# Kernel optimization log

Measured on AMD Instinct MI355X. Metric: run time of the kernel, lower is better.

Reference implementation:

```python
import jax, jax.numpy as jnp
import numpy as np

N_NODES = 50000
N_EDGES = 800000
IN_CH = 128
OUT_CH = 64
HEADS = 2
NEG_SLOPE = 0.2


def _gat_conv(x, src, dst, W, a_src, a_dst, b, n):
    """PyG-style GATConv (eval mode: no dropout), self-loops already appended.
    x: [n, F_in]; W: [F_in, H*C]; a_src/a_dst: [H, C]; b: [H*C]."""
    H, C = a_src.shape
    h = (x @ W).reshape(n, H, C)                       # [n, H, C]
    alpha_src = jnp.sum(h * a_src, axis=-1)            # [n, H]
    alpha_dst = jnp.sum(h * a_dst, axis=-1)            # [n, H]
    e = alpha_src[src] + alpha_dst[dst]                # [E, H]
    e = jnp.where(e > 0, e, NEG_SLOPE * e)             # LeakyReLU(0.2)
    # neighbor-wise (destination-grouped) softmax, numerically stable
    m = jax.ops.segment_max(e, dst, num_segments=n)
    e = jnp.exp(e - m[dst])
    denom = jax.ops.segment_sum(e, dst, num_segments=n)
    alpha = e / (denom[dst] + 1e-16)                   # [E, H]
    out = jax.ops.segment_sum(alpha[:, :, None] * h[src], dst, num_segments=n)
    return out.reshape(n, H * C) + b


def setup_inputs() -> dict:
    key = jax.random.key(0)
    ks = jax.random.split(key, 12)
    s = 0.08  # glorot-ish scale
    x = jax.random.normal(ks[0], (N_NODES, IN_CH), dtype=jnp.float32)
    edge_index = jax.random.randint(ks[1], (2, N_EDGES), 0, N_NODES, dtype=jnp.int64)
    H, O = HEADS, OUT_CH
    return {
        "x": x,
        "edge_index": edge_index,
        "W1": jax.random.normal(ks[2], (IN_CH, H * 2 * O), dtype=jnp.float32) * s,
        "a_src1": jax.random.normal(ks[3], (H, 2 * O), dtype=jnp.float32) * s,
        "a_dst1": jax.random.normal(ks[4], (H, 2 * O), dtype=jnp.float32) * s,
        "b1": jnp.zeros((H * 2 * O,), dtype=jnp.float32),
        "W_mu": jax.random.normal(ks[5], (2 * O * H, H * O), dtype=jnp.float32) * s,
        "a_src_mu": jax.random.normal(ks[6], (H, O), dtype=jnp.float32) * s,
        "a_dst_mu": jax.random.normal(ks[7], (H, O), dtype=jnp.float32) * s,
        "b_mu": jnp.zeros((H * O,), dtype=jnp.float32),
        "W_ls": jax.random.normal(ks[8], (2 * O * H, H * O), dtype=jnp.float32) * s,
        "a_src_ls": jax.random.normal(ks[9], (H, O), dtype=jnp.float32) * s,
        "a_dst_ls": jax.random.normal(ks[10], (H, O), dtype=jnp.float32) * s,
        "b_ls": jnp.zeros((H * O,), dtype=jnp.float32),
    }


def reference(x, edge_index, W1, a_src1, a_dst1, b1,
              W_mu, a_src_mu, a_dst_mu, b_mu,
              W_ls, a_src_ls, a_dst_ls, b_ls):
    n = x.shape[0]
    loop = jnp.arange(n, dtype=edge_index.dtype)
    src = jnp.concatenate([edge_index[0], loop])  # PyG add_self_loops=True
    dst = jnp.concatenate([edge_index[1], loop])
    x1 = jax.nn.elu(_gat_conv(x, src, dst, W1, a_src1, a_dst1, b1, n))
    mu = _gat_conv(x1, src, dst, W_mu, a_src_mu, a_dst_mu, b_mu, n)
    logstd = _gat_conv(x1, src, dst, W_ls, a_src_ls, a_dst_ls, b_ls, n)
    return (mu, logstd)
```

## Files before the change

kernel.cpp:

```cpp
#include <hip/hip_runtime.h>


typedef unsigned short u16;
typedef unsigned int u32;
typedef _Float16 f16;
typedef f16 f16x8 __attribute__((ext_vector_type(8)));
typedef float f32x4v __attribute__((ext_vector_type(4)));

__device__ __forceinline__ u16 f2h(float f) {
    union { f16 h; u16 u; } t;
    t.h = (f16)f;
    return t.u;
}
__device__ __forceinline__ float4 loadh4(const u16* __restrict__ p, size_t i) {
    union { uint2 u; f16 h[4]; } t;
    t.u = *(const uint2*)(p + i);
    return make_float4((float)t.h[0], (float)t.h[1], (float)t.h[2], (float)t.h[3]);
}
__device__ __forceinline__ void store4(float* __restrict__ p, size_t i, float4 v) {
    *(float4*)(p + i) = v;
}
__device__ __forceinline__ void store4(u16* __restrict__ p, size_t i, float4 v) {
    union { uint2 u; f16 h[4]; } t;
    t.h[0] = (f16)v.x; t.h[1] = (f16)v.y; t.h[2] = (f16)v.z; t.h[3] = (f16)v.w;
    *(uint2*)(p + i) = t.u;
}

__global__ __launch_bounds__(256) void k_detect(const u32* __restrict__ ebuf,
                                                int* __restrict__ flag) {
    __shared__ int nz;
    if (threadIdx.x == 0) nz = 0;
    __syncthreads();
    if (ebuf[2 * threadIdx.x + 1] != 0u) atomicAdd(&nz, 1);
    __syncthreads();
    if (threadIdx.x == 0) *flag = (nz == 0) ? 1 : 0;
}

__global__ __launch_bounds__(256) void k_extract(const u32* __restrict__ ebuf, int E,
                                                 const int* __restrict__ flag,
                                                 int* __restrict__ se,
                                                 int* __restrict__ de,
                                                 int* __restrict__ deg) {
    int e = blockIdx.x * 256 + threadIdx.x;
    if (e >= E) return;
    int s, d;
    if (*flag) {
        s = (int)ebuf[2 * (size_t)e];
        d = (int)ebuf[2 * ((size_t)E + (size_t)e)];
    } else {
        s = (int)ebuf[e];
        d = (int)ebuf[(size_t)E + (size_t)e];
    }
    se[e] = s;
    de[e] = d;
    atomicAdd(&deg[d], 1);
}

__global__ __launch_bounds__(256) void k_scan_a(const int* __restrict__ deg, int n,
                                                int* __restrict__ bsum) {
    __shared__ int s[256];
    int i = blockIdx.x * 256 + threadIdx.x;
    s[threadIdx.x] = (i < n) ? deg[i] : 0;
    __syncthreads();
    for (int st = 128; st > 0; st >>= 1) {
        if (threadIdx.x < st) s[threadIdx.x] += s[threadIdx.x + st];
        __syncthreads();
    }
    if (threadIdx.x == 0) bsum[blockIdx.x] = s[0];
}

__global__ __launch_bounds__(256) void k_scan_b(int* __restrict__ bsum, int nb) {
    __shared__ int s[256];
    int t = threadIdx.x;
    int v = (t < nb) ? bsum[t] : 0;
    s[t] = v;
    __syncthreads();
    for (int off = 1; off < 256; off <<= 1) {
        int add = (t >= off) ? s[t - off] : 0;
        __syncthreads();
        s[t] += add;
        __syncthreads();
    }
    if (t < nb) bsum[t] = s[t] - v;
}

__global__ __launch_bounds__(256) void k_scan_c(const int* __restrict__ deg, int n,
                                                const int* __restrict__ bsum,
                                                int* __restrict__ rowptr,
                                                int* __restrict__ cursor, int E) {
    __shared__ int s[256];
    int t = threadIdx.x;
    int i = blockIdx.x * 256 + t;
    int v = (i < n) ? deg[i] : 0;
    s[t] = v;
    __syncthreads();
    for (int off = 1; off < 256; off <<= 1) {
        int add = (t >= off) ? s[t - off] : 0;
        __syncthreads();
        s[t] += add;
        __syncthreads();
    }
    if (i < n) {
        int ex = bsum[blockIdx.x] + s[t] - v;
        rowptr[i] = ex;
        cursor[i] = ex;
    }
    if (i == 0) rowptr[n] = E;
}

__global__ __launch_bounds__(256) void k_fill(const int* __restrict__ src,
                                              const int* __restrict__ dst, int E,
                                              int* __restrict__ cursor,
                                              int* __restrict__ csr_src) {
    int e = blockIdx.x * 256 + threadIdx.x;
    if (e < E) {
        int d = dst[e];
        int slot = atomicAdd(&cursor[d], 1);
        csr_src[slot] = src[e];
    }
}

__global__ __launch_bounds__(256) void k_cvt(const float* __restrict__ in,
                                             u16* __restrict__ out, int nElem) {
    int i = (blockIdx.x * 256 + threadIdx.x) * 4;
    if (i >= nElem) return;
    float4 v = *(const float4*)(in + i);
    store4(out, i, v);
}

__global__ __launch_bounds__(256) void k_tw(const float* __restrict__ Wl,
                                            const float* __restrict__ Wr, int split,
                                            int K, u16* __restrict__ Wt) {
    int idx = blockIdx.x * 256 + threadIdx.x;
    if (idx >= 256 * K) return;
    int c = idx / K, k = idx - c * K;
    float v;
    if (split == 256)
        v = Wl[(size_t)k * 256 + c];
    else
        v = (c < 128) ? Wl[(size_t)k * 128 + c] : Wr[(size_t)k * 128 + (c - 128)];
    Wt[idx] = f2h(v);
}

template <int K, int ALOGW>
__global__ __launch_bounds__(256) void k_gemm_mfma(
    const u16* __restrict__ Ah, const u16* __restrict__ Wt, u16* __restrict__ out,
    float* __restrict__ as_out, float* __restrict__ ad_out,
    const float* __restrict__ alo, const float* __restrict__ ahi,
    const float* __restrict__ dlo, const float* __restrict__ dhi, int M) {
    __shared__ u16 Bs[256 * 40];
    const int tid = threadIdx.x;
    const int wave = tid >> 6;
    const int lane = tid & 63;
    const int li = lane & 15;
    const int quad = lane >> 4;
    const int r0 = blockIdx.x * 64 + wave * 16;
    int arowi = r0 + li;
    if (arowi >= M) arowi = M - 1;
    const u16* arow = Ah + (size_t)arowi * K + quad * 8;

    f32x4v acc[16];
#pragma unroll
    for (int ct = 0; ct < 16; ct++) acc[ct] = (f32x4v)(0.f);

    for (int t = 0; t < K; t += 32) {
        __syncthreads();
        {
            const u16* src = Wt + (size_t)tid * K + t;
            u16* dst = Bs + tid * 40;
            uint4 v0 = ((const uint4*)src)[0];
            uint4 v1 = ((const uint4*)src)[1];
            uint4 v2 = ((const uint4*)src)[2];
            uint4 v3 = ((const uint4*)src)[3];
            ((uint4*)dst)[0] = v0;
            ((uint4*)(dst + 8))[0] = v1;
            ((uint4*)(dst + 16))[0] = v2;
            ((uint4*)(dst + 24))[0] = v3;
        }
        __syncthreads();
        f16x8 a = *(const f16x8*)(arow + t);
#pragma unroll
        for (int ct = 0; ct < 16; ct++) {
            f16x8 b = *(const f16x8*)(Bs + (ct * 16 + li) * 40 + quad * 8);
            acc[ct] = __builtin_amdgcn_mfma_f32_16x16x32_f16(a, b, acc[ct], 0, 0, 0);
        }
    }

#pragma unroll
    for (int reg = 0; reg < 4; reg++) {
        int grow = r0 + quad * 4 + reg;
        if (grow < M) {
            u16* orow = out + (size_t)grow * 256 + li;
#pragma unroll
            for (int ct = 0; ct < 16; ct++) orow[ct * 16] = f2h(acc[ct][reg]);
        }
    }

    const int NS = 64 >> ALOGW;
    const int SH = ALOGW - 2;
    float aw[16], dw[16];
#pragma unroll
    for (int ct = 0; ct < 16; ct++) {
        int col = ct * 16 + li;
        aw[ct] = (col < 128) ? alo[col] : ahi[col - 128];
        dw[ct] = (col < 128) ? dlo[col] : dhi[col - 128];
    }
#pragma unroll
    for (int reg = 0; reg < 4; reg++) {
        float s[4] = {0.f, 0.f, 0.f, 0.f};
        float d[4] = {0.f, 0.f, 0.f, 0.f};
#pragma unroll
        for (int ct = 0; ct < 16; ct++) {
            int sl = ct >> SH;
            s[sl] += acc[ct][reg] * aw[ct];
            d[sl] += acc[ct][reg] * dw[ct];
        }
#pragma unroll
        for (int sl = 0; sl < NS; sl++) {
#pragma unroll
            for (int m = 1; m <= 8; m <<= 1) {
                s[sl] += __shfl_xor(s[sl], m, 64);
                d[sl] += __shfl_xor(d[sl], m, 64);
            }
        }
        int grow = r0 + quad * 4 + reg;
        if (li == 0 && grow < M) {
#pragma unroll
            for (int sl = 0; sl < NS; sl++) {
                as_out[(size_t)grow * NS + sl] = s[sl];
                ad_out[(size_t)grow * NS + sl] = d[sl];
            }
        }
    }
}

template <int LOGW, int MODE, typename OT>
__global__ __launch_bounds__(256) void k_agg(const u16* __restrict__ h,
                                             const int* __restrict__ rowptr,
                                             const int* __restrict__ csr_src,
                                             const float* __restrict__ as,
                                             const float* __restrict__ ad,
                                             const float* __restrict__ b_lo,
                                             const float* __restrict__ b_hi,
                                             OT* __restrict__ outp, int n) {
    const int NS = 64 >> LOGW;
    int wid = blockIdx.x * 4 + (threadIdx.x >> 6);
    int lane = threadIdx.x & 63;
    if (wid >= n) return;
    int slot = lane >> LOGW;
    int c = lane * 4;

    float adv = ad[(size_t)wid * NS + slot];
    float e = as[(size_t)wid * NS + slot] + adv;
    e = fmaxf(e, 0.2f * e);
    float w = __expf(e);
    float denom = w;
    float4 hv = loadh4(h, (size_t)wid * 256 + c);
    float acc0 = w * hv.x, acc1 = w * hv.y, acc2 = w * hv.z, acc3 = w * hv.w;

    const int rb = rowptr[wid], re = rowptr[wid + 1];
    int p = rb;
    for (; p + 4 <= re; p += 4) {
        int s0 = csr_src[p], s1 = csr_src[p + 1];
        int s2 = csr_src[p + 2], s3 = csr_src[p + 3];
        float e0 = as[(size_t)s0 * NS + slot] + adv;
        float e1 = as[(size_t)s1 * NS + slot] + adv;
        float e2 = as[(size_t)s2 * NS + slot] + adv;
        float e3 = as[(size_t)s3 * NS + slot] + adv;
        e0 = fmaxf(e0, 0.2f * e0);
        e1 = fmaxf(e1, 0.2f * e1);
        e2 = fmaxf(e2, 0.2f * e2);
        e3 = fmaxf(e3, 0.2f * e3);
        float w0 = __expf(e0), w1 = __expf(e1), w2 = __expf(e2), w3 = __expf(e3);
        float4 h0 = loadh4(h, (size_t)s0 * 256 + c);
        float4 h1 = loadh4(h, (size_t)s1 * 256 + c);
        float4 h2 = loadh4(h, (size_t)s2 * 256 + c);
        float4 h3 = loadh4(h, (size_t)s3 * 256 + c);
        denom += (w0 + w1) + (w2 + w3);
        acc0 += w0 * h0.x + w1 * h1.x + w2 * h2.x + w3 * h3.x;
        acc1 += w0 * h0.y + w1 * h1.y + w2 * h2.y + w3 * h3.y;
        acc2 += w0 * h0.z + w1 * h1.z + w2 * h2.z + w3 * h3.z;
        acc3 += w0 * h0.w + w1 * h1.w + w2 * h2.w + w3 * h3.w;
    }
    for (; p < re; ++p) {
        int s = csr_src[p];
        float ev = as[(size_t)s * NS + slot] + adv;
        ev = fmaxf(ev, 0.2f * ev);
        float ww = __expf(ev);
        denom += ww;
        float4 hh = loadh4(h, (size_t)s * 256 + c);
        acc0 += ww * hh.x;
        acc1 += ww * hh.y;
        acc2 += ww * hh.z;
        acc3 += ww * hh.w;
    }
    float inv = 1.0f / (denom + 1e-16f);

    int ci = c & 127;
    const float* bp = (c < 128) ? b_lo : b_hi;
    float4 bv = *(const float4*)(bp + ci);
    float v0 = acc0 * inv + bv.x;
    float v1 = acc1 * inv + bv.y;
    float v2 = acc2 * inv + bv.z;
    float v3 = acc3 * inv + bv.w;

    if (MODE == 0) {
        v0 = v0 > 0.f ? v0 : expm1f(v0);
        v1 = v1 > 0.f ? v1 : expm1f(v1);
        v2 = v2 > 0.f ? v2 : expm1f(v2);
        v3 = v3 > 0.f ? v3 : expm1f(v3);
        store4(outp, (size_t)wid * 256 + c, make_float4(v0, v1, v2, v3));
    } else {
        size_t base = (c < 128) ? ((size_t)wid * 128 + c)
                                : ((size_t)n * 128 + (size_t)wid * 128 + (c - 128));
        store4(outp, base, make_float4(v0, v1, v2, v3));
    }
}

extern "C" void kernel_launch(void* const* d_in, const int* in_sizes, int n_in,
                              void* d_out, int out_size, void* d_ws, size_t ws_size,
                              hipStream_t stream) {
    const float* x = (const float*)d_in[0];
    const u32* ebuf = (const u32*)d_in[1];
    const float* W1 = (const float*)d_in[2];
    const float* a_src1 = (const float*)d_in[3];
    const float* a_dst1 = (const float*)d_in[4];
    const float* b1 = (const float*)d_in[5];
    const float* W_mu = (const float*)d_in[6];
    const float* a_src_mu = (const float*)d_in[7];
    const float* a_dst_mu = (const float*)d_in[8];
    const float* b_mu = (const float*)d_in[9];
    const float* W_ls = (const float*)d_in[10];
    const float* a_src_ls = (const float*)d_in[11];
    const float* a_dst_ls = (const float*)d_in[12];
    const float* b_ls = (const float*)d_in[13];

    const int n = in_sizes[0] / 128;
    const int E = in_sizes[1] / 2;

    char* base = (char*)d_ws;
    size_t off = 0;
    auto alloc = [&](size_t b) -> char* {
        char* p = base + off;
        off = (off + b + 255) & ~(size_t)255;
        return p;
    };
    int* rowptr = (int*)alloc((size_t)(n + 1) * 4);
    int* cursor = (int*)alloc((size_t)n * 4);
    int* csr = (int*)alloc((size_t)E * 4);
    int* bsum = (int*)alloc(256 * 4);
    int* eflag = (int*)alloc(256);
    int* se = (int*)alloc((size_t)E * 4);
    int* de = (int*)alloc((size_t)E * 4);
    float* as = (float*)alloc((size_t)n * 4 * 4);
    float* ad = (float*)alloc((size_t)n * 4 * 4);
    u16* W1t = (u16*)alloc(256 * 128 * 2);
    u16* Wt2 = (u16*)alloc(256 * 256 * 2);
    u16* x1h = (u16*)alloc((size_t)n * 256 * 2);
    u16* xh = x1h;
    u16* h = (u16*)alloc((size_t)n * 256 * 2);

    const int nb = (n + 255) / 256;
    const int eg = (E + 255) / 256;
    const int ng4 = (n + 3) / 4;
    const int gg = (n + 63) / 64;

    hipMemsetAsync(cursor, 0, (size_t)n * 4, stream);
    k_detect<<<1, 256, 0, stream>>>(ebuf, eflag);
    k_extract<<<eg, 256, 0, stream>>>(ebuf, E, eflag, se, de, cursor);
    k_scan_a<<<nb, 256, 0, stream>>>(cursor, n, bsum);
    k_scan_b<<<1, 256, 0, stream>>>(bsum, nb);
    k_scan_c<<<nb, 256, 0, stream>>>(cursor, n, bsum, rowptr, cursor, E);
    k_fill<<<eg, 256, 0, stream>>>(se, de, E, cursor, csr);

    k_cvt<<<(n * 128 / 4 + 255) / 256, 256, 0, stream>>>(x, xh, n * 128);
    k_tw<<<(256 * 128 + 255) / 256, 256, 0, stream>>>(W1, W1, 256, 128, W1t);
    k_tw<<<(256 * 256 + 255) / 256, 256, 0, stream>>>(W_mu, W_ls, 128, 256, Wt2);

    k_gemm_mfma<128, 5><<<gg, 256, 0, stream>>>(xh, W1t, h, as, ad, a_src1,
                                                a_src1 + 128, a_dst1, a_dst1 + 128,
                                                n);
    k_agg<5, 0, u16><<<ng4, 256, 0, stream>>>(h, rowptr, csr, as, ad, b1, b1 + 128,
                                              x1h, n);

    k_gemm_mfma<256, 4><<<gg, 256, 0, stream>>>(x1h, Wt2, h, as, ad, a_src_mu,
                                                a_src_ls, a_dst_mu, a_dst_ls, n);
    k_agg<4, 1, float><<<ng4, 256, 0, stream>>>(h, rowptr, csr, as, ad, b_mu, b_ls,
                                                (float*)d_out, n);
}
```

Measured before the change: 383.2 us.

## Split aggregation columns into halves mapped to XCD groups for L2 locality

The aggregation kernel now splits each node's 256 feature columns into two halves handled by separate blocks. Blocks are mapped so that XCDs 0-3 process the low half and XCDs 4-7 the high half, so each XCD's L2 caches only half of every gathered h row. The intent is to raise the L2 hit rate on random neighbour gathers. The cost is twice as many blocks, each gathering only 4 bytes per lane, and the attention logits and CSR indices are recomputed or re-read by both halves.

Result: slower. 417.2 us (+8.9%).

```diff
diff --git a/kernel.cpp b/kernel.cpp
--- a/kernel.cpp
+++ b/kernel.cpp
@@ -12,10 +12,17 @@
     t.h = (f16)f;
     return t.u;
 }
-__device__ __forceinline__ float4 loadh4(const u16* __restrict__ p, size_t i) {
-    union { uint2 u; f16 h[4]; } t;
-    t.u = *(const uint2*)(p + i);
-    return make_float4((float)t.h[0], (float)t.h[1], (float)t.h[2], (float)t.h[3]);
+__device__ __forceinline__ float2 loadh2(const u16* __restrict__ p, size_t i) {
+    union { u32 u; f16 h[2]; } t;
+    t.u = *(const u32*)(p + i);
+    return make_float2((float)t.h[0], (float)t.h[1]);
+}
+__device__ __forceinline__ void store2h(u16* __restrict__ p, size_t i, float a,
+                                        float b) {
+    union { u32 u; f16 h[2]; } t;
+    t.h[0] = (f16)a;
+    t.h[1] = (f16)b;
+    *(u32*)(p + i) = t.u;
 }
 __device__ __forceinline__ void store4(float* __restrict__ p, size_t i, float4 v) {
     *(float4*)(p + i) = v;
@@ -235,28 +242,34 @@
 }
 
 template <int LOGW, int MODE, typename OT>
-__global__ __launch_bounds__(256) void k_agg(const u16* __restrict__ h,
-                                             const int* __restrict__ rowptr,
-                                             const int* __restrict__ csr_src,
-                                             const float* __restrict__ as,
-                                             const float* __restrict__ ad,
-                                             const float* __restrict__ b_lo,
-                                             const float* __restrict__ b_hi,
-                                             OT* __restrict__ outp, int n) {
+__global__ __launch_bounds__(256) void k_agg2(const u16* __restrict__ h,
+                                              const int* __restrict__ rowptr,
+                                              const int* __restrict__ csr_src,
+                                              const float* __restrict__ as,
+                                              const float* __restrict__ ad,
+                                              const float* __restrict__ b_lo,
+                                              const float* __restrict__ b_hi,
+                                              OT* __restrict__ outp, int n,
+                                              int nGrp) {
     const int NS = 64 >> LOGW;
-    int wid = blockIdx.x * 4 + (threadIdx.x >> 6);
-    int lane = threadIdx.x & 63;
+    const int bid = blockIdx.x;
+    const int xcd = bid & 7;
+    const int half = xcd >> 2;
+    const int grp = (bid >> 3) * 4 + (xcd & 3);
+    if (grp >= nGrp) return;
+    const int wid = grp * 4 + (threadIdx.x >> 6);
     if (wid >= n) return;
-    int slot = lane >> LOGW;
-    int c = lane * 4;
+    const int lane = threadIdx.x & 63;
+    const int col = half * 128 + lane * 2;
+    const int slot = col >> (LOGW + 2);
 
     float adv = ad[(size_t)wid * NS + slot];
     float e = as[(size_t)wid * NS + slot] + adv;
     e = fmaxf(e, 0.2f * e);
     float w = __expf(e);
     float denom = w;
-    float4 hv = loadh4(h, (size_t)wid * 256 + c);
-    float acc0 = w * hv.x, acc1 = w * hv.y, acc2 = w * hv.z, acc3 = w * hv.w;
+    float2 hv = loadh2(h, (size_t)wid * 256 + col);
+    float acc0 = w * hv.x, acc1 = w * hv.y;
 
     const int rb = rowptr[wid], re = rowptr[wid + 1];
     int p = rb;
@@ -272,15 +285,13 @@
         e2 = fmaxf(e2, 0.2f * e2);
         e3 = fmaxf(e3, 0.2f * e3);
         float w0 = __expf(e0), w1 = __expf(e1), w2 = __expf(e2), w3 = __expf(e3);
-        float4 h0 = loadh4(h, (size_t)s0 * 256 + c);
-        float4 h1 = loadh4(h, (size_t)s1 * 256 + c);
-        float4 h2 = loadh4(h, (size_t)s2 * 256 + c);
-        float4 h3 = loadh4(h, (size_t)s3 * 256 + c);
+        float2 h0 = loadh2(h, (size_t)s0 * 256 + col);
+        float2 h1 = loadh2(h, (size_t)s1 * 256 + col);
+        float2 h2 = loadh2(h, (size_t)s2 * 256 + col);
+        float2 h3 = loadh2(h, (size_t)s3 * 256 + col);
         denom += (w0 + w1) + (w2 + w3);
         acc0 += w0 * h0.x + w1 * h1.x + w2 * h2.x + w3 * h3.x;
         acc1 += w0 * h0.y + w1 * h1.y + w2 * h2.y + w3 * h3.y;
-        acc2 += w0 * h0.z + w1 * h1.z + w2 * h2.z + w3 * h3.z;
-        acc3 += w0 * h0.w + w1 * h1.w + w2 * h2.w + w3 * h3.w;
     }
     for (; p < re; ++p) {
         int s = csr_src[p];
@@ -288,32 +299,26 @@
         ev = fmaxf(ev, 0.2f * ev);
         float ww = __expf(ev);
         denom += ww;
-        float4 hh = loadh4(h, (size_t)s * 256 + c);
+        float2 hh = loadh2(h, (size_t)s * 256 + col);
         acc0 += ww * hh.x;
         acc1 += ww * hh.y;
-        acc2 += ww * hh.z;
-        acc3 += ww * hh.w;
     }
     float inv = 1.0f / (denom + 1e-16f);
 
-    int ci = c & 127;
-    const float* bp = (c < 128) ? b_lo : b_hi;
-    float4 bv = *(const float4*)(bp + ci);
+    const float* bp = half ? b_hi : b_lo;
+    const int ci = lane * 2;
+    float2 bv = *(const float2*)(bp + ci);
     float v0 = acc0 * inv + bv.x;
     float v1 = acc1 * inv + bv.y;
-    float v2 = acc2 * inv + bv.z;
-    float v3 = acc3 * inv + bv.w;
 
     if (MODE == 0) {
         v0 = v0 > 0.f ? v0 : expm1f(v0);
         v1 = v1 > 0.f ? v1 : expm1f(v1);
-        v2 = v2 > 0.f ? v2 : expm1f(v2);
-        v3 = v3 > 0.f ? v3 : expm1f(v3);
-        store4(outp, (size_t)wid * 256 + c, make_float4(v0, v1, v2, v3));
+        store2h((u16*)outp, (size_t)wid * 256 + col, v0, v1);
     } else {
-        size_t base = (c < 128) ? ((size_t)wid * 128 + c)
-                                : ((size_t)n * 128 + (size_t)wid * 128 + (c - 128));
-        store4(outp, base, make_float4(v0, v1, v2, v3));
+        size_t base = half ? ((size_t)n * 128 + (size_t)wid * 128 + ci)
+                           : ((size_t)wid * 128 + ci);
+        *(float2*)((float*)outp + base) = make_float2(v0, v1);
     }
 }
 
@@ -362,8 +367,9 @@
 
     const int nb = (n + 255) / 256;
     const int eg = (E + 255) / 256;
-    const int ng4 = (n + 3) / 4;
     const int gg = (n + 63) / 64;
+    const int nGrp = (n + 3) / 4;
+    const int aggGrid = 8 * ((nGrp + 3) / 4);
 
     hipMemsetAsync(cursor, 0, (size_t)n * 4, stream);
     k_detect<<<1, 256, 0, stream>>>(ebuf, eflag);
@@ -380,11 +386,11 @@
     k_gemm_mfma<128, 5><<<gg, 256, 0, stream>>>(xh, W1t, h, as, ad, a_src1,
                                                 a_src1 + 128, a_dst1, a_dst1 + 128,
                                                 n);
-    k_agg<5, 0, u16><<<ng4, 256, 0, stream>>>(h, rowptr, csr, as, ad, b1, b1 + 128,
-                                              x1h, n);
+    k_agg2<5, 0, u16><<<aggGrid, 256, 0, stream>>>(h, rowptr, csr, as, ad, b1,
+                                                   b1 + 128, x1h, n, nGrp);
 
     k_gemm_mfma<256, 4><<<gg, 256, 0, stream>>>(x1h, Wt2, h, as, ad, a_src_mu,
                                                 a_src_ls, a_dst_mu, a_dst_ls, n);
-    k_agg<4, 1, float><<<ng4, 256, 0, stream>>>(h, rowptr, csr, as, ad, b_mu, b_ls,
-                                                (float*)d_out, n);
-}
+    k_agg2<4, 1, float><<<aggGrid, 256, 0, stream>>>(h, rowptr, csr, as, ad, b_mu,
+                                                     b_ls, (float*)d_out, n, nGrp);
+}
```

## Split aggregation feature columns across XCD halves for per-XCD L2 locality

Applied to the files above, without the earlier changes.

The aggregation kernel now assigns each half-wave to one destination node and only half of the 256 feature columns. Block ids are mapped so that XCDs 0-3 handle the low 128 columns and XCDs 4-7 the high 128 columns. The aim is to halve the gathered h working set per XCD so that random neighbor gathers hit in each XCD's private L2 more often. In exchange, CSR indices and attention scalars are read twice (once per half), and each node's edge loop runs on two half-waves. The kernel also relies on round-robin block-to-XCD dispatch.

Result: no change. 388.1 us (+1.3%).

```diff
diff --git a/kernel.cpp b/kernel.cpp
--- a/kernel.cpp
+++ b/kernel.cpp
@@ -235,30 +235,40 @@
 }
 
 template <int LOGW, int MODE, typename OT>
-__global__ __launch_bounds__(256) void k_agg(const u16* __restrict__ h,
-                                             const int* __restrict__ rowptr,
-                                             const int* __restrict__ csr_src,
-                                             const float* __restrict__ as,
-                                             const float* __restrict__ ad,
-                                             const float* __restrict__ b_lo,
-                                             const float* __restrict__ b_hi,
-                                             OT* __restrict__ outp, int n) {
+__global__ __launch_bounds__(256) void k_agg3(const u16* __restrict__ h,
+                                              const int* __restrict__ rowptr,
+                                              const int* __restrict__ csr_src,
+                                              const float* __restrict__ as,
+                                              const float* __restrict__ ad,
+                                              const float* __restrict__ b_lo,
+                                              const float* __restrict__ b_hi,
+                                              OT* __restrict__ outp, int n,
+                                              int nGrp) {
     const int NS = 64 >> LOGW;
-    int wid = blockIdx.x * 4 + (threadIdx.x >> 6);
-    int lane = threadIdx.x & 63;
-    if (wid >= n) return;
-    int slot = lane >> LOGW;
-    int c = lane * 4;
+    const int bid = blockIdx.x;
+    const int xcd = bid & 7;
+    const int half = xcd >> 2;
+    const int grp = (bid >> 3) * 4 + (xcd & 3);
+    if (grp >= nGrp) return;
+    const int lane = threadIdx.x & 63;
+    const int sub = lane >> 5;
+    const int sl = lane & 31;
+    const int wid0 = grp * 8 + (threadIdx.x >> 6) * 2 + sub;
+    const bool ok = wid0 < n;
+    const int wid = ok ? wid0 : (n - 1);
+    const int col = half * 128 + sl * 4;
+    const int slot = col >> (LOGW + 2);
 
     float adv = ad[(size_t)wid * NS + slot];
     float e = as[(size_t)wid * NS + slot] + adv;
     e = fmaxf(e, 0.2f * e);
     float w = __expf(e);
     float denom = w;
-    float4 hv = loadh4(h, (size_t)wid * 256 + c);
+    float4 hv = loadh4(h, (size_t)wid * 256 + col);
     float acc0 = w * hv.x, acc1 = w * hv.y, acc2 = w * hv.z, acc3 = w * hv.w;
 
-    const int rb = rowptr[wid], re = rowptr[wid + 1];
+    int rb = 0, re = 0;
+    if (ok) { rb = rowptr[wid0]; re = rowptr[wid0 + 1]; }
     int p = rb;
     for (; p + 4 <= re; p += 4) {
         int s0 = csr_src[p], s1 = csr_src[p + 1];
@@ -272,10 +282,10 @@
         e2 = fmaxf(e2, 0.2f * e2);
         e3 = fmaxf(e3, 0.2f * e3);
         float w0 = __expf(e0), w1 = __expf(e1), w2 = __expf(e2), w3 = __expf(e3);
-        float4 h0 = loadh4(h, (size_t)s0 * 256 + c);
-        float4 h1 = loadh4(h, (size_t)s1 * 256 + c);
-        float4 h2 = loadh4(h, (size_t)s2 * 256 + c);
-        float4 h3 = loadh4(h, (size_t)s3 * 256 + c);
+        float4 h0 = loadh4(h, (size_t)s0 * 256 + col);
+        float4 h1 = loadh4(h, (size_t)s1 * 256 + col);
+        float4 h2 = loadh4(h, (size_t)s2 * 256 + col);
+        float4 h3 = loadh4(h, (size_t)s3 * 256 + col);
         denom += (w0 + w1) + (w2 + w3);
         acc0 += w0 * h0.x + w1 * h1.x + w2 * h2.x + w3 * h3.x;
         acc1 += w0 * h0.y + w1 * h1.y + w2 * h2.y + w3 * h3.y;
@@ -288,7 +298,7 @@
         ev = fmaxf(ev, 0.2f * ev);
         float ww = __expf(ev);
         denom += ww;
-        float4 hh = loadh4(h, (size_t)s * 256 + c);
+        float4 hh = loadh4(h, (size_t)s * 256 + col);
         acc0 += ww * hh.x;
         acc1 += ww * hh.y;
         acc2 += ww * hh.z;
@@ -296,24 +306,25 @@
     }
     float inv = 1.0f / (denom + 1e-16f);
 
-    int ci = c & 127;
-    const float* bp = (c < 128) ? b_lo : b_hi;
+    const float* bp = half ? b_hi : b_lo;
+    const int ci = sl * 4;
     float4 bv = *(const float4*)(bp + ci);
     float v0 = acc0 * inv + bv.x;
     float v1 = acc1 * inv + bv.y;
     float v2 = acc2 * inv + bv.z;
     float v3 = acc3 * inv + bv.w;
 
+    if (!ok) return;
     if (MODE == 0) {
         v0 = v0 > 0.f ? v0 : expm1f(v0);
         v1 = v1 > 0.f ? v1 : expm1f(v1);
         v2 = v2 > 0.f ? v2 : expm1f(v2);
         v3 = v3 > 0.f ? v3 : expm1f(v3);
-        store4(outp, (size_t)wid * 256 + c, make_float4(v0, v1, v2, v3));
+        store4((u16*)outp, (size_t)wid0 * 256 + col, make_float4(v0, v1, v2, v3));
     } else {
-        size_t base = (c < 128) ? ((size_t)wid * 128 + c)
-                                : ((size_t)n * 128 + (size_t)wid * 128 + (c - 128));
-        store4(outp, base, make_float4(v0, v1, v2, v3));
+        size_t base = half ? ((size_t)n * 128 + (size_t)wid0 * 128 + ci)
+                           : ((size_t)wid0 * 128 + ci);
+        store4((float*)outp, base, make_float4(v0, v1, v2, v3));
     }
 }
 
@@ -362,8 +373,9 @@
 
     const int nb = (n + 255) / 256;
     const int eg = (E + 255) / 256;
-    const int ng4 = (n + 3) / 4;
     const int gg = (n + 63) / 64;
+    const int nGrp = (n + 7) / 8;
+    const int aggGrid = 8 * ((nGrp + 3) / 4);
 
     hipMemsetAsync(cursor, 0, (size_t)n * 4, stream);
     k_detect<<<1, 256, 0, stream>>>(ebuf, eflag);
@@ -380,11 +392,11 @@
     k_gemm_mfma<128, 5><<<gg, 256, 0, stream>>>(xh, W1t, h, as, ad, a_src1,
                                                 a_src1 + 128, a_dst1, a_dst1 + 128,
                                                 n);
-    k_agg<5, 0, u16><<<ng4, 256, 0, stream>>>(h, rowptr, csr, as, ad, b1, b1 + 128,
-                                              x1h, n);
+    k_agg3<5, 0, u16><<<aggGrid, 256, 0, stream>>>(h, rowptr, csr, as, ad, b1,
+                                                   b1 + 128, x1h, n, nGrp);
 
     k_gemm_mfma<256, 4><<<gg, 256, 0, stream>>>(x1h, Wt2, h, as, ad, a_src_mu,
                                                 a_src_ls, a_dst_mu, a_dst_ls, n);
-    k_agg<4, 1, float><<<ng4, 256, 0, stream>>>(h, rowptr, csr, as, ad, b_mu, b_ls,
-                                                (float*)d_out, n);
-}
+    k_agg3<4, 1, float><<<aggGrid, 256, 0, stream>>>(h, rowptr, csr, as, ad, b_mu,
+                                                     b_ls, (float*)d_out, n, nGrp);
+}
```
